# Kernel optimization log

Measured on AMD Instinct MI355X. Metric: run time of the kernel, lower is better.

## Reference

```python
import jax, jax.numpy as jnp
import numpy as np

B, N, D = 2, 2048, 1024
H, DH = 16, 64
FF = 4096


def _layernorm(x, g, b, eps=1e-5):
    mu = jnp.mean(x, axis=-1, keepdims=True)
    var = jnp.var(x, axis=-1, keepdims=True)
    return (x - mu) * jax.lax.rsqrt(var + eps) * g + b


def setup_inputs() -> dict:
    key = jax.random.key(0)
    ks = jax.random.split(key, 8)
    s = 0.02  # realistic init scale so softmax is well-behaved
    return {
        "x": jax.random.normal(ks[0], (B, N, D), jnp.float32),
        "wq": jax.random.normal(ks[1], (D, H * DH), jnp.float32) * s,
        "wk": jax.random.normal(ks[2], (D, H * DH), jnp.float32) * s,
        "wv": jax.random.normal(ks[3], (D, H * DH), jnp.float32) * s,
        "wo": jax.random.normal(ks[4], (H * DH, D), jnp.float32) * s,
        "w1": jax.random.normal(ks[5], (D, FF), jnp.float32) * s,
        "b1": jnp.zeros((FF,), jnp.float32),
        "w2": jax.random.normal(ks[6], (FF, D), jnp.float32) * s,
        "b2": jnp.zeros((D,), jnp.float32),
        "ln1_g": jnp.ones((D,), jnp.float32),
        "ln1_b": jnp.zeros((D,), jnp.float32),
        "ln2_g": jnp.ones((D,), jnp.float32),
        "ln2_b": jnp.zeros((D,), jnp.float32),
    }


def reference(x, wq, wk, wv, wo, w1, b1, w2, b2, ln1_g, ln1_b, ln2_g, ln2_b):
    # --- pre-norm self-attention (encoder path, no masks/mem/topk) ---
    res = x
    h = _layernorm(x, ln1_g, ln1_b)
    q = (h @ wq).reshape(B, N, H, DH).transpose(0, 2, 1, 3)  # b h n d
    k = (h @ wk).reshape(B, N, H, DH).transpose(0, 2, 1, 3)
    v = (h @ wv).reshape(B, N, H, DH).transpose(0, 2, 1, 3)
    # NOTE: source has NO 1/sqrt(d) scaling
    dots = jnp.einsum("bhid,bhjd->bhij", q, k)
    attn = jax.nn.softmax(dots.astype(jnp.float32), axis=-1).astype(dots.dtype)
    out = jnp.einsum("bhij,bhjd->bhid", attn, v)
    out = out.transpose(0, 2, 1, 3).reshape(B, N, H * DH) @ wo
    x = out + res
    # --- pre-norm feedforward (exact GELU) ---
    res = x
    h = _layernorm(x, ln2_g, ln2_b)
    h = jax.nn.gelu(h @ w1 + b1, approximate=False)
    x = (h @ w2 + b2) + res
    return x
```

## Files before the change

kernel.cpp:

```cpp
#include <hip/hip_runtime.h>
#include <math.h>
#include <stdint.h>

#define B_  2
#define N_  2048
#define D_  1024
#define H_  16
#define DH_ 64
#define FF_ 4096
#define M_  (B_ * N_)

typedef __bf16 bf16;
typedef float  f32x4  __attribute__((ext_vector_type(4)));
typedef __bf16 bf16x8 __attribute__((ext_vector_type(8)));
typedef __bf16 bf16x4 __attribute__((ext_vector_type(4)));
typedef __bf16 bf16x2 __attribute__((ext_vector_type(2)));

__device__ __forceinline__ void async_copy16(const void* g, void* l) {
    __builtin_amdgcn_global_load_lds((__attribute__((address_space(1))) unsigned int*)g,
                                     (__attribute__((address_space(3))) unsigned int*)l,
                                     16, 0, 0);
}

__global__ __launch_bounds__(256) void ln_kernel(const float* __restrict__ x,
                                                 const float* __restrict__ g,
                                                 const float* __restrict__ bta,
                                                 bf16* __restrict__ y)
{
    const int row = blockIdx.x;
    const int t = threadIdx.x;
    const float4 v = ((const float4*)(x + (size_t)row * D_))[t];
    float s  = v.x + v.y + v.z + v.w;
    float s2 = v.x * v.x + v.y * v.y + v.z * v.z + v.w * v.w;
#pragma unroll
    for (int o = 32; o > 0; o >>= 1) {
        s  += __shfl_down(s, o);
        s2 += __shfl_down(s2, o);
    }
    __shared__ float red[8];
    const int wid = t >> 6;
    if ((t & 63) == 0) { red[wid] = s; red[4 + wid] = s2; }
    __syncthreads();
    if (t == 0) {
        red[0] = red[0] + red[1] + red[2] + red[3];
        red[4] = red[4] + red[5] + red[6] + red[7];
    }
    __syncthreads();
    const float mean = red[0] * (1.0f / D_);
    const float var  = red[4] * (1.0f / D_) - mean * mean;
    const float rstd = rsqrtf(var + 1e-5f);
    const float4 gg = ((const float4*)g)[t];
    const float4 bb = ((const float4*)bta)[t];
    bf16x4 o;
    o[0] = (bf16)((v.x - mean) * rstd * gg.x + bb.x);
    o[1] = (bf16)((v.y - mean) * rstd * gg.y + bb.y);
    o[2] = (bf16)((v.z - mean) * rstd * gg.z + bb.z);
    o[3] = (bf16)((v.w - mean) * rstd * gg.w + bb.w);
    ((bf16x4*)(y + (size_t)row * D_))[t] = o;
}

__global__ __launch_bounds__(256) void transpose_bf16(const float* __restrict__ in,
                                                      bf16* __restrict__ out,
                                                      int R, int C)
{
    __shared__ float tile[32][33];
    const int c0 = blockIdx.x * 32, r0 = blockIdx.y * 32;
    const int tx = threadIdx.x, ty = threadIdx.y;
#pragma unroll
    for (int i = 0; i < 4; i++)
        tile[ty + i * 8][tx] = in[(size_t)(r0 + ty + i * 8) * C + c0 + tx];
    __syncthreads();
#pragma unroll
    for (int i = 0; i < 4; i++)
        out[(size_t)(c0 + ty + i * 8) * R + r0 + tx] = (bf16)tile[tx][ty + i * 8];
}

__global__ __launch_bounds__(256) void transpose3_bf16(const float* __restrict__ a,
                                                       const float* __restrict__ b,
                                                       const float* __restrict__ c,
                                                       bf16* __restrict__ out)
{
    __shared__ float tile[32][33];
    const float* in = (blockIdx.z == 0) ? a : (blockIdx.z == 1) ? b : c;
    bf16* o = out + (size_t)blockIdx.z * D_ * D_;
    const int c0 = blockIdx.x * 32, r0 = blockIdx.y * 32;
    const int tx = threadIdx.x, ty = threadIdx.y;
#pragma unroll
    for (int i = 0; i < 4; i++)
        tile[ty + i * 8][tx] = in[(size_t)(r0 + ty + i * 8) * D_ + c0 + tx];
    __syncthreads();
#pragma unroll
    for (int i = 0; i < 4; i++)
        o[(size_t)(c0 + ty + i * 8) * D_ + r0 + tx] = (bf16)tile[tx][ty + i * 8];
}

template <int EPI, int OMODE>
__global__ __launch_bounds__(256) void mfma_gemm(const bf16* __restrict__ A,
                                                 const bf16* __restrict__ Bt,
                                                 void* __restrict__ Cout,
                                                 int M, int N, int K,
                                                 const float* __restrict__ bias,
                                                 const float* __restrict__ res)
{
    __shared__ bf16 As[128 * 32];
    __shared__ bf16 Bs[128 * 32];
    const int t = threadIdx.x;
    const int w = t >> 6, lane = t & 63;
    const int wr = w >> 1, wc = w & 1;
    const int m0 = blockIdx.y * 128, n0 = blockIdx.x * 128;
    const int lr = lane & 15, lg = lane >> 4;
    const size_t MDc = (size_t)M_ * D_;

    f32x4 acc[4][4];
#pragma unroll
    for (int m = 0; m < 4; m++)
#pragma unroll
        for (int n = 0; n < 4; n++) acc[m][n] = {0.f, 0.f, 0.f, 0.f};

    const int q0c = w * 2, q1c = w * 2 + 1;
    const int row0 = q0c * 16 + (lane >> 2);
    const int row1 = q1c * 16 + (lane >> 2);
    const int kk = (lane & 3) * 8;

    for (int k0 = 0; k0 < K; k0 += 32) {
        async_copy16(A  + (size_t)(m0 + row0) * K + k0 + kk, &As[q0c * 512]);
        async_copy16(A  + (size_t)(m0 + row1) * K + k0 + kk, &As[q1c * 512]);
        async_copy16(Bt + (size_t)(n0 + row0) * K + k0 + kk, &Bs[q0c * 512]);
        async_copy16(Bt + (size_t)(n0 + row1) * K + k0 + kk, &Bs[q1c * 512]);
        __syncthreads();

        bf16x8 af[4], bfr[4];
#pragma unroll
        for (int m = 0; m < 4; m++)
            af[m] = *(const bf16x8*)&As[(wr * 64 + m * 16 + lr) * 32 + lg * 8];
#pragma unroll
        for (int n = 0; n < 4; n++)
            bfr[n] = *(const bf16x8*)&Bs[(wc * 64 + n * 16 + lr) * 32 + lg * 8];
#pragma unroll
        for (int m = 0; m < 4; m++)
#pragma unroll
            for (int n = 0; n < 4; n++)
                acc[m][n] = __builtin_amdgcn_mfma_f32_16x16x32_bf16(
                    af[m], bfr[n], acc[m][n], 0, 0, 0);
        __syncthreads();
    }

#pragma unroll
    for (int m = 0; m < 4; m++)
#pragma unroll
        for (int n = 0; n < 4; n++) {
            const int col = n0 + wc * 64 + n * 16 + lr;
            const float bv = (EPI >= 2) ? bias[col] : 0.f;
            if (OMODE == 3) {
                const int slice = col >> 10;
                const int c = col & 1023;
                if (slice == 2) {
                    const int head = c >> 6, dh = c & 63;
                    const int row0_ = m0 + wr * 64 + m * 16 + lg * 4;
                    const int bb = row0_ >> 11, nn = row0_ & 2047;
                    bf16x4 st;
#pragma unroll
                    for (int r2 = 0; r2 < 4; r2++) st[r2] = (bf16)acc[m][n][r2];
                    *(bf16x4*)((bf16*)Cout + 2 * MDc +
                               (size_t)((bb * H_ + head) * DH_ + dh) * N_ + nn) = st;
                } else {
                    bf16* dst = (bf16*)Cout + (size_t)slice * MDc;
#pragma unroll
                    for (int r2 = 0; r2 < 4; r2++) {
                        const int row = m0 + wr * 64 + m * 16 + lg * 4 + r2;
                        dst[(size_t)row * D_ + c] = (bf16)acc[m][n][r2];
                    }
                }
            } else {
#pragma unroll
                for (int r2 = 0; r2 < 4; r2++) {
                    const int row = m0 + wr * 64 + m * 16 + lg * 4 + r2;
                    float v = acc[m][n][r2] + bv;
                    if (EPI == 1 || EPI == 3) v += res[(size_t)row * N + col];
                    if (EPI == 2) v = 0.5f * v * (1.0f + erff(v * 0.70710678118654752f));
                    if (OMODE == 1) ((bf16*)Cout)[(size_t)row * N + col] = (bf16)v;
                    else            ((float*)Cout)[(size_t)row * N + col] = v;
                }
            }
        }
}

__global__ __launch_bounds__(512, 4) void mfma_attn(const bf16* __restrict__ Q,
                                                    const bf16* __restrict__ K,
                                                    const bf16* __restrict__ Vt,
                                                    bf16* __restrict__ O)
{
    const int qt = blockIdx.x, h = blockIdx.y, b = blockIdx.z;
    const int t = threadIdx.x, w = t >> 6, lane = t & 63;
    const int lr = lane & 15, lg = lane >> 4;

    __shared__ bf16 Ks[2][64 * 64];
    __shared__ bf16 Vs[2][64 * 64];
    __shared__ bf16 Ps[8][16 * 72];

    const int q0w = qt * 128 + w * 16;
    bf16x8 b_q[2];
#pragma unroll
    for (int ki = 0; ki < 2; ki++)
        b_q[ki] = *(const bf16x8*)&Q[(size_t)(b * N_ + q0w + lr) * (H_ * DH_)
                                     + h * DH_ + ki * 32 + lg * 8];

    f32x4 acc[4];
#pragma unroll
    for (int nd = 0; nd < 4; nd++) acc[nd] = {0.f, 0.f, 0.f, 0.f};
    float m_run = -3.0e38f, l_run = 0.f;

    const int srow = lane >> 3;
    const int schunk = (lane & 7) ^ srow;
    const int r_st = w * 8 + srow;

    auto stage = [&](int kv0, int buf) {
        async_copy16(&K[(size_t)(b * N_ + kv0 + r_st) * (H_ * DH_) + h * DH_ + schunk * 8],
                     &Ks[buf][w * 8 * 64]);
        async_copy16(&Vt[((size_t)(b * H_ + h) * DH_ + r_st) * N_ + kv0 + schunk * 8],
                     &Vs[buf][w * 8 * 64]);
    };

    stage(0, 0);
    const int NT = N_ / 64;
    for (int it = 0; it < NT; ++it) {
        __syncthreads();
        if (it + 1 < NT) stage((it + 1) * 64, (it + 1) & 1);
        const bf16* ks = Ks[it & 1];
        const bf16* vs = Vs[it & 1];

        f32x4 s[4];
#pragma unroll
        for (int ni = 0; ni < 4; ni++) s[ni] = {0.f, 0.f, 0.f, 0.f};
        __builtin_amdgcn_s_setprio(1);
#pragma unroll
        for (int ki = 0; ki < 2; ki++)
#pragma unroll
            for (int ni = 0; ni < 4; ni++) {
                const int r = ni * 16 + lr;
                const int slot = (lg + ki * 4) ^ (r & 7);
                const bf16x8 bk = *(const bf16x8*)&ks[r * 64 + slot * 8];
                s[ni] = __builtin_amdgcn_mfma_f32_16x16x32_bf16(
                    bk, b_q[ki], s[ni], 0, 0, 0);
            }
        __builtin_amdgcn_s_setprio(0);

        float pmax = s[0][0];
#pragma unroll
        for (int ni = 0; ni < 4; ni++)
#pragma unroll
            for (int r2 = 0; r2 < 4; r2++)
                pmax = fmaxf(pmax, s[ni][r2]);
        pmax = fmaxf(pmax, __shfl_xor(pmax, 16));
        pmax = fmaxf(pmax, __shfl_xor(pmax, 32));
        const float mn = fmaxf(m_run, pmax);
        const float resc = __expf(m_run - mn);
        m_run = mn;

        float p[4][4];
        float rsum = 0.f;
#pragma unroll
        for (int ni = 0; ni < 4; ni++)
#pragma unroll
            for (int r2 = 0; r2 < 4; r2++) {
                p[ni][r2] = __expf(s[ni][r2] - mn);
                rsum += p[ni][r2];
            }
        rsum += __shfl_xor(rsum, 16);
        rsum += __shfl_xor(rsum, 32);
        l_run = l_run * resc + rsum;
#pragma unroll
        for (int nd = 0; nd < 4; nd++)
#pragma unroll
            for (int r2 = 0; r2 < 4; r2++) acc[nd][r2] *= resc;

#pragma unroll
        for (int ni = 0; ni < 4; ni++)
#pragma unroll
            for (int hh = 0; hh < 2; hh++) {
                bf16x2 pr;
                pr[0] = (bf16)p[ni][2 * hh + 0];
                pr[1] = (bf16)p[ni][2 * hh + 1];
                *(bf16x2*)&Ps[w][lr * 72 + ni * 16 + lg * 4 + hh * 2] = pr;
            }

        __builtin_amdgcn_s_setprio(1);
#pragma unroll
        for (int k2 = 0; k2 < 2; k2++) {
            const bf16x8 bp = *(const bf16x8*)&Ps[w][lr * 72 + k2 * 32 + lg * 8];
#pragma unroll
            for (int nd = 0; nd < 4; nd++) {
                const int r = nd * 16 + lr;
                const int slot = (lg + k2 * 4) ^ (r & 7);
                const bf16x8 av = *(const bf16x8*)&vs[r * 64 + slot * 8];
                acc[nd] = __builtin_amdgcn_mfma_f32_16x16x32_bf16(
                    av, bp, acc[nd], 0, 0, 0);
            }
        }
        __builtin_amdgcn_s_setprio(0);
    }

    const float inv = 1.f / l_run;
    const size_t obase = (size_t)(b * N_ + q0w + lr) * (H_ * DH_) + h * DH_;
#pragma unroll
    for (int nd = 0; nd < 4; nd++) {
        bf16x4 o4;
#pragma unroll
        for (int r2 = 0; r2 < 4; r2++) o4[r2] = (bf16)(acc[nd][r2] * inv);
        *(bf16x4*)&O[obase + nd * 16 + lg * 4] = o4;
    }
}

extern "C" void kernel_launch(void* const* d_in, const int* in_sizes, int n_in,
                              void* d_out, int out_size, void* d_ws, size_t ws_size,
                              hipStream_t stream)
{
    const float* x     = (const float*)d_in[0];
    const float* wq    = (const float*)d_in[1];
    const float* wk    = (const float*)d_in[2];
    const float* wv    = (const float*)d_in[3];
    const float* wo    = (const float*)d_in[4];
    const float* w1    = (const float*)d_in[5];
    const float* b1    = (const float*)d_in[6];
    const float* w2    = (const float*)d_in[7];
    const float* b2    = (const float*)d_in[8];
    const float* ln1_g = (const float*)d_in[9];
    const float* ln1_b = (const float*)d_in[10];
    const float* ln2_g = (const float*)d_in[11];
    const float* ln2_b = (const float*)d_in[12];

    const size_t MD = (size_t)M_ * D_;
    char* wsb = (char*)d_ws;
    auto alloc = [&](size_t bytes) { char* p = wsb; wsb += (bytes + 255) & ~(size_t)255; return p; };
    bf16*  hb    = (bf16*)alloc(MD * 2);
    bf16*  qb    = (bf16*)alloc(MD * 2 * 3);
    bf16*  kb    = qb + MD;
    bf16*  vtb   = qb + 2 * MD;
    bf16*  ab    = (bf16*)alloc(MD * 2);
    float* x1    = (float*)alloc(MD * 4);
    bf16*  h2b   = (bf16*)alloc(MD * 2);
    bf16*  ffb   = (bf16*)alloc((size_t)M_ * FF_ * 2);
    bf16*  wqkvT = (bf16*)alloc((size_t)3 * D_ * D_ * 2);
    bf16*  woT   = (bf16*)alloc((size_t)D_ * D_ * 2);
    bf16*  w1T   = (bf16*)alloc((size_t)D_ * FF_ * 2);
    bf16*  w2T   = (bf16*)alloc((size_t)FF_ * D_ * 2);

    dim3 tb(32, 8);
    transpose3_bf16<<<dim3(D_ / 32, D_ / 32, 3), tb, 0, stream>>>(wq, wk, wv, wqkvT);
    transpose_bf16<<<dim3(D_ / 32, D_ / 32), tb, 0, stream>>>(wo, woT, D_, D_);
    transpose_bf16<<<dim3(FF_ / 32, D_ / 32), tb, 0, stream>>>(w1, w1T, D_, FF_);
    transpose_bf16<<<dim3(D_ / 32, FF_ / 32), tb, 0, stream>>>(w2, w2T, FF_, D_);

    ln_kernel<<<M_, 256, 0, stream>>>(x, ln1_g, ln1_b, hb);

    mfma_gemm<0, 3><<<dim3(3 * D_ / 128, M_ / 128), 256, 0, stream>>>(
        hb, wqkvT, qb, M_, 3 * D_, D_, nullptr, nullptr);

    mfma_attn<<<dim3(N_ / 128, H_, B_), 512, 0, stream>>>(qb, kb, vtb, ab);

    dim3 gP(D_ / 128, M_ / 128);
    mfma_gemm<1, 0><<<gP, 256, 0, stream>>>(ab, woT, x1, M_, D_, D_, nullptr, x);

    ln_kernel<<<M_, 256, 0, stream>>>(x1, ln2_g, ln2_b, h2b);

    mfma_gemm<2, 1><<<dim3(FF_ / 128, M_ / 128), 256, 0, stream>>>(
        h2b, w1T, ffb, M_, FF_, D_, b1, nullptr);

    mfma_gemm<3, 0><<<dim3(D_ / 128, M_ / 128), 256, 0, stream>>>(
        ffb, w2T, (float*)d_out, M_, D_, FF_, b2, x1);
}
```

Baseline: 420.7 us.

## Split-K the FF2 GEMM with a reduce kernel and swizzle GEMM block order

Every MFMA GEMM now remaps its flat block index with a stride-8 swizzle, so neighbouring tiles land on the same XCD and should reuse the L2 cache better. The final FF2 GEMM (K=4096) is split into two K halves over blockIdx.z. Each half writes fp32 partials into reused workspace, and a new reduce kernel adds the partials, bias and residual. This doubles the block count for a grid that previously had only 256 blocks. The cost is 32MB of extra fp32 partial traffic and one more kernel launch.

```diff
diff --git a/kernel.cpp b/kernel.cpp
--- a/kernel.cpp
+++ b/kernel.cpp
@@ -98,7 +98,7 @@
 __global__ __launch_bounds__(256) void mfma_gemm(const bf16* __restrict__ A,
                                                  const bf16* __restrict__ Bt,
                                                  void* __restrict__ Cout,
-                                                 int M, int N, int K,
+                                                 int M, int N, int K, int kspl,
                                                  const float* __restrict__ bias,
                                                  const float* __restrict__ res)
 {
@@ -107,7 +107,15 @@
     const int t = threadIdx.x;
     const int w = t >> 6, lane = t & 63;
     const int wr = w >> 1, wc = w & 1;
-    const int m0 = blockIdx.y * 128, n0 = blockIdx.x * 128;
+
+    const unsigned nwg = gridDim.x * gridDim.y;
+    const unsigned lid = blockIdx.y * gridDim.x + blockIdx.x;
+    const unsigned q = nwg >> 3;
+    const unsigned swz = (lid & 7) * q + (lid >> 3);
+    const int bx = swz % gridDim.x, by = swz / gridDim.x;
+    const int ks = blockIdx.z;
+
+    const int m0 = by * 128, n0 = bx * 128;
     const int lr = lane & 15, lg = lane >> 4;
     const size_t MDc = (size_t)M_ * D_;
 
@@ -122,7 +130,8 @@
     const int row1 = q1c * 16 + (lane >> 2);
     const int kk = (lane & 3) * 8;
 
-    for (int k0 = 0; k0 < K; k0 += 32) {
+    const int kbeg = ks * kspl, kend = kbeg + kspl;
+    for (int k0 = kbeg; k0 < kend; k0 += 32) {
         async_copy16(A  + (size_t)(m0 + row0) * K + k0 + kk, &As[q0c * 512]);
         async_copy16(A  + (size_t)(m0 + row1) * K + k0 + kk, &As[q1c * 512]);
         async_copy16(Bt + (size_t)(n0 + row0) * K + k0 + kk, &Bs[q0c * 512]);
@@ -150,8 +159,15 @@
 #pragma unroll
         for (int n = 0; n < 4; n++) {
             const int col = n0 + wc * 64 + n * 16 + lr;
-            const float bv = (EPI >= 2) ? bias[col] : 0.f;
-            if (OMODE == 3) {
+            const float bv = (EPI >= 2 && OMODE != 4) ? bias[col] : 0.f;
+            if (OMODE == 4) {
+                float* dst = (float*)Cout + (size_t)ks * M * N;
+#pragma unroll
+                for (int r2 = 0; r2 < 4; r2++) {
+                    const int row = m0 + wr * 64 + m * 16 + lg * 4 + r2;
+                    dst[(size_t)row * N + col] = acc[m][n][r2];
+                }
+            } else if (OMODE == 3) {
                 const int slice = col >> 10;
                 const int c = col & 1023;
                 if (slice == 2) {
@@ -183,6 +199,25 @@
                 }
             }
         }
+}
+
+__global__ __launch_bounds__(256) void reduce2_kernel(const float* __restrict__ p0,
+                                                      const float* __restrict__ p1,
+                                                      const float* __restrict__ bias,
+                                                      const float* __restrict__ res,
+                                                      float* __restrict__ out)
+{
+    const size_t idx = ((size_t)blockIdx.x * 256 + threadIdx.x) * 4;
+    const float4 a = *(const float4*)(p0 + idx);
+    const float4 b = *(const float4*)(p1 + idx);
+    const float4 r = *(const float4*)(res + idx);
+    const float4 bb = *(const float4*)(bias + (idx & (D_ - 1)));
+    float4 o;
+    o.x = a.x + b.x + r.x + bb.x;
+    o.y = a.y + b.y + r.y + bb.y;
+    o.z = a.z + b.z + r.z + bb.z;
+    o.w = a.w + b.w + r.w + bb.w;
+    *(float4*)(out + idx) = o;
 }
 
 __global__ __launch_bounds__(512, 4) void mfma_attn(const bf16* __restrict__ Q,
@@ -344,6 +379,8 @@
     bf16*  woT   = (bf16*)alloc((size_t)D_ * D_ * 2);
     bf16*  w1T   = (bf16*)alloc((size_t)D_ * FF_ * 2);
     bf16*  w2T   = (bf16*)alloc((size_t)FF_ * D_ * 2);
+    float* part0 = (float*)d_ws;
+    float* part1 = part0 + MD;
 
     dim3 tb(32, 8);
     transpose3_bf16<<<dim3(D_ / 32, D_ / 32, 3), tb, 0, stream>>>(wq, wk, wv, wqkvT);
@@ -354,18 +391,20 @@
     ln_kernel<<<M_, 256, 0, stream>>>(x, ln1_g, ln1_b, hb);
 
     mfma_gemm<0, 3><<<dim3(3 * D_ / 128, M_ / 128), 256, 0, stream>>>(
-        hb, wqkvT, qb, M_, 3 * D_, D_, nullptr, nullptr);
+        hb, wqkvT, qb, M_, 3 * D_, D_, D_, nullptr, nullptr);
 
     mfma_attn<<<dim3(N_ / 128, H_, B_), 512, 0, stream>>>(qb, kb, vtb, ab);
 
     dim3 gP(D_ / 128, M_ / 128);
-    mfma_gemm<1, 0><<<gP, 256, 0, stream>>>(ab, woT, x1, M_, D_, D_, nullptr, x);
+    mfma_gemm<1, 0><<<gP, 256, 0, stream>>>(ab, woT, x1, M_, D_, D_, D_, nullptr, x);
 
     ln_kernel<<<M_, 256, 0, stream>>>(x1, ln2_g, ln2_b, h2b);
 
     mfma_gemm<2, 1><<<dim3(FF_ / 128, M_ / 128), 256, 0, stream>>>(
-        h2b, w1T, ffb, M_, FF_, D_, b1, nullptr);
-
-    mfma_gemm<3, 0><<<dim3(D_ / 128, M_ / 128), 256, 0, stream>>>(
-        ffb, w2T, (float*)d_out, M_, D_, FF_, b2, x1);
-}
+        h2b, w1T, ffb, M_, FF_, D_, D_, b1, nullptr);
+
+    mfma_gemm<0, 4><<<dim3(D_ / 128, M_ / 128, 2), 256, 0, stream>>>(
+        ffb, w2T, part0, M_, D_, FF_, FF_ / 2, nullptr, nullptr);
+    reduce2_kernel<<<MD / (256 * 4), 256, 0, stream>>>(
+        part0, part1, b2, x1, (float*)d_out);
+}
```

Measured after the change: 407.5 us. 3.1% less time.
